# Kernel tuning notes

Hardware: AMD Instinct MI355X
Metric: run time of the kernel (lower is better)

The kernel has to match this reference:

```python
import jax, jax.numpy as jnp
import numpy as np

N_NODES = 50000
N_EDGES = 800000
HIDDEN = 128
HEADS = 8
HEAD_DIM = HIDDEN // HEADS
N_REL = 64
SCALE = np.sqrt(HEAD_DIM).astype(np.float32)


def setup_inputs() -> dict:
    key = jax.random.key(0)
    ks = jax.random.split(key, 12)
    s = 1.0 / np.sqrt(2 * HIDDEN)
    s2 = 1.0 / np.sqrt(HIDDEN)
    return {
        "node_features": jax.random.normal(ks[0], (N_NODES, HIDDEN), jnp.float32),
        "query_embedding": jax.random.normal(ks[1], (1, HIDDEN), jnp.float32),
        "relation_embeddings": jax.random.normal(ks[2], (N_REL, HIDDEN), jnp.float32),
        "Wq": jax.random.uniform(ks[3], (2 * HIDDEN, HIDDEN), jnp.float32, -s, s),
        "bq": jnp.zeros((HIDDEN,), jnp.float32),
        "Wk": jax.random.uniform(ks[4], (2 * HIDDEN, HIDDEN), jnp.float32, -s, s),
        "bk": jnp.zeros((HIDDEN,), jnp.float32),
        "Wv": jax.random.uniform(ks[5], (HIDDEN, HIDDEN), jnp.float32, -s2, s2),
        "bv": jnp.zeros((HIDDEN,), jnp.float32),
        "Wo": jax.random.uniform(ks[6], (HIDDEN, HIDDEN), jnp.float32, -s2, s2),
        "bo": jnp.zeros((HIDDEN,), jnp.float32),
        "edge_index": jax.random.randint(ks[7], (2, N_EDGES), 0, N_NODES, jnp.int64),
        "edge_type": jax.random.randint(ks[8], (N_EDGES,), 0, N_REL, jnp.int64),
    }


def reference(node_features, query_embedding, relation_embeddings,
              Wq, bq, Wk, bk, Wv, bv, Wo, bo, edge_index, edge_type):
    n = node_features.shape[0]
    # expand query to all nodes and concat: [N, 2*hidden]
    q_exp = jnp.broadcast_to(query_embedding, (n, HIDDEN))
    nq = jnp.concatenate([node_features, q_exp], axis=-1)
    q = (nq @ Wq + bq).reshape(n, HEADS, HEAD_DIM)
    k = (nq @ Wk + bk).reshape(n, HEADS, HEAD_DIM)
    v = (node_features @ Wv + bv).reshape(n, HEADS, HEAD_DIM)

    src, dst = edge_index[0], edge_index[1]
    rel_bias = relation_embeddings[edge_type].reshape(-1, HEADS, HEAD_DIM)

    # edge-wise scores [E, heads]
    scores = jnp.sum(q[dst] * (k[src] + rel_bias), axis=-1) / SCALE

    # sparse softmax grouped by dst; torch init of max buffer is 0 -> clamp at 0
    seg_max = jax.ops.segment_max(scores, dst, num_segments=n)
    seg_max = jnp.maximum(seg_max, 0.0)
    exp_s = jnp.exp(scores - seg_max[dst])
    seg_sum = jax.ops.segment_sum(exp_s, dst, num_segments=n)
    attn = exp_s / (seg_sum[dst] + 1e-8)  # [E, heads]

    messages = attn[:, :, None] * v[src]  # [E, heads, head_dim]
    out = jax.ops.segment_sum(messages, dst, num_segments=n)  # [N, heads, head_dim]
    out = out.reshape(n, HIDDEN)
    return out @ Wo + bo
```

## Files before the change

### kernel.cpp

```cpp
#include <hip/hip_runtime.h>
#include <math.h>

#define N_NODES 50000
#define N_EDGES 800000
#define HID 128
#define HEADS 8
#define HDIM 16
#define CNT_BLOCKS 3125
#define QKV_BLOCKS 782

typedef __attribute__((ext_vector_type(8))) short short8;
typedef __attribute__((ext_vector_type(4))) float floatx4;

#if defined(__has_builtin)
#if __has_builtin(__builtin_amdgcn_fdot2_f32_bf16)
#define HAVE_DOT2 1
#endif
#endif
#ifndef HAVE_DOT2
#define HAVE_DOT2 0
#endif

#if HAVE_DOT2
typedef __attribute__((ext_vector_type(2))) __bf16 bf16x2;
__device__ __forceinline__ float dot2acc(unsigned int a, unsigned int b, float c) {
    return __builtin_amdgcn_fdot2_f32_bf16(__builtin_bit_cast(bf16x2, a),
                                           __builtin_bit_cast(bf16x2, b), c, false);
}
#endif

__device__ __forceinline__ float bf_lo(unsigned int d) { return __uint_as_float(d << 16); }
__device__ __forceinline__ float bf_hi(unsigned int d) { return __uint_as_float(d & 0xFFFF0000u); }
__device__ __forceinline__ unsigned short f2bf(float f) {
    unsigned int u = __float_as_uint(f);
    u = (u + 0x7FFFu + ((u >> 16) & 1u)) >> 16;
    return (unsigned short)u;
}
__device__ __forceinline__ unsigned int pack_bf2(float a, float b) {
    return (unsigned int)f2bf(a) | ((unsigned int)f2bf(b) << 16);
}

__global__ __launch_bounds__(256) void prep_count_kernel(
    const float* __restrict__ query, const float* __restrict__ rel,
    const float* __restrict__ Wq, const float* __restrict__ bq,
    const float* __restrict__ Wk, const float* __restrict__ bk,
    const float* __restrict__ Wv, const float* __restrict__ Wo,
    const int* __restrict__ ei,
    unsigned short* __restrict__ Wt, unsigned short* __restrict__ relbf,
    int* __restrict__ counts, int* __restrict__ epos,
    float* __restrict__ bqe, float* __restrict__ bke) {
    int b = blockIdx.x;
    if (b < CNT_BLOCKS) {
        int e = b * 256 + threadIdx.x;
        if (e < N_EDGES) epos[e] = atomicAdd(&counts[ei[N_EDGES + e]], 1);
        return;
    }
    b -= CNT_BLOCKS;
    if (b == 256) {
        int j = threadIdx.x;
        if (j < HID) {
            float aq = bq[j], ak = bk[j];
            for (int i = 0; i < HID; ++i) {
                float qv = query[i];
                aq += qv * Wq[(HID + i) * HID + j];
                ak += qv * Wk[(HID + i) * HID + j];
            }
            bqe[j] = aq;
            bke[j] = ak;
        }
        return;
    }
    int idx = b * 256 + threadIdx.x;
    if (idx < 64 * HID) relbf[idx] = f2bf(rel[idx]);
    int m = idx >> 14;
    int rem = idx & 16383;
    int n = rem >> 7, k = rem & 127;
    const float* W = (m == 0) ? Wq : (m == 1) ? Wk : (m == 2) ? Wv : Wo;
    Wt[idx] = f2bf(W[k * HID + n]);
}

__global__ __launch_bounds__(256) void scan1_kernel(const int* __restrict__ counts,
                                                    int* __restrict__ row_start,
                                                    int* __restrict__ bsums) {
    __shared__ int wsum[4];
    int b = blockIdx.x, tid = threadIdx.x, lane = tid & 63, w = tid >> 6;
    int i0 = b * 1024 + tid * 4;
    int x0 = (i0 + 0 < N_NODES) ? counts[i0 + 0] : 0;
    int x1 = (i0 + 1 < N_NODES) ? counts[i0 + 1] : 0;
    int x2 = (i0 + 2 < N_NODES) ? counts[i0 + 2] : 0;
    int x3 = (i0 + 3 < N_NODES) ? counts[i0 + 3] : 0;
    int t = x0 + x1 + x2 + x3;
    int val = t;
    #pragma unroll
    for (int off = 1; off < 64; off <<= 1) {
        int y = __shfl_up(val, off);
        if (lane >= off) val += y;
    }
    if (lane == 63) wsum[w] = val;
    __syncthreads();
    int wo = 0;
    if (w > 0) wo += wsum[0];
    if (w > 1) wo += wsum[1];
    if (w > 2) wo += wsum[2];
    int excl = wo + val - t;
    if (i0 + 0 < N_NODES) row_start[i0 + 0] = excl;
    if (i0 + 1 < N_NODES) row_start[i0 + 1] = excl + x0;
    if (i0 + 2 < N_NODES) row_start[i0 + 2] = excl + x0 + x1;
    if (i0 + 3 < N_NODES) row_start[i0 + 3] = excl + x0 + x1 + x2;
    if (tid == 255) bsums[b] = wo + val;
}

__global__ __launch_bounds__(256) void scan23_kernel(int* __restrict__ row_start,
                                                     const int* __restrict__ bsums) {
    __shared__ int soff;
    int b = blockIdx.x, tid = threadIdx.x;
    if (tid < 64) {
        int x = (tid < b) ? bsums[tid] : 0;
        #pragma unroll
        for (int off = 32; off > 0; off >>= 1) x += __shfl_down(x, off);
        if (tid == 0) soff = x;
    }
    __syncthreads();
    int off = soff;
    int i0 = b * 1024 + tid * 4;
    if (i0 + 3 < N_NODES) {
        int4* p = (int4*)(row_start + i0);
        int4 v = *p;
        v.x += off; v.y += off; v.z += off; v.w += off;
        *p = v;
    } else {
        for (int j = 0; j < 4; ++j)
            if (i0 + j < N_NODES) row_start[i0 + j] += off;
    }
    if (b == 0 && tid == 0) row_start[N_NODES] = N_EDGES;
}

__global__ __launch_bounds__(256) void qkv_scatter_kernel(
    const float* __restrict__ nf, const unsigned short* __restrict__ Wt,
    const float* __restrict__ bqe, const float* __restrict__ bke, const float* __restrict__ bv,
    const int* __restrict__ ei, const int* __restrict__ et,
    const int* __restrict__ row_start, const int* __restrict__ epos,
    unsigned short* __restrict__ qb16, unsigned short* __restrict__ kv16,
    unsigned int* __restrict__ csr) {
    if (blockIdx.x >= QKV_BLOCKS) {
        int e = (blockIdx.x - QKV_BLOCKS) * 256 + threadIdx.x;
        if (e < N_EDGES) {
            int dst = ei[N_EDGES + e];
            csr[row_start[dst] + epos[e]] = ((unsigned int)et[e] << 18) | (unsigned int)ei[e];
        }
        return;
    }
    int row0 = blockIdx.x * 64;
    int wave = threadIdx.x >> 6;
    int lane = threadIdx.x & 63;
    int col  = lane & 15;
    int quad = lane >> 4;

    short8 afr[4][4];
    #pragma unroll
    for (int t = 0; t < 4; ++t) {
        int arow = row0 + t * 16 + col;
        int asafe = (arow < N_NODES) ? arow : (N_NODES - 1);
        #pragma unroll
        for (int kk = 0; kk < 4; ++kk) {
            const float4* ap = (const float4*)(nf + (size_t)asafe * HID + kk * 32 + quad * 8);
            float4 a0 = ap[0], a1 = ap[1];
            short8 f;
            f[0] = (short)f2bf(a0.x); f[1] = (short)f2bf(a0.y);
            f[2] = (short)f2bf(a0.z); f[3] = (short)f2bf(a0.w);
            f[4] = (short)f2bf(a1.x); f[5] = (short)f2bf(a1.y);
            f[6] = (short)f2bf(a1.z); f[7] = (short)f2bf(a1.w);
            afr[t][kk] = f;
        }
    }

    const float* biases[3] = {bqe, bke, bv};
    #pragma unroll
    for (int m = 0; m < 3; ++m) {
        const unsigned short* W = Wt + (size_t)m * HID * HID;
        #pragma unroll
        for (int nn = 0; nn < 2; ++nn) {
            int n = wave * 2 + nn;
            float b = biases[m][n * 16 + col];
            floatx4 acc[4];
            #pragma unroll
            for (int t = 0; t < 4; ++t) acc[t] = (floatx4){b, b, b, b};
            short8 bfr[4];
            #pragma unroll
            for (int kk = 0; kk < 4; ++kk)
                bfr[kk] = *(const short8*)(W + (size_t)(n * 16 + col) * HID + kk * 32 + quad * 8);
            #pragma unroll
            for (int kk = 0; kk < 4; ++kk)
                #pragma unroll
                for (int t = 0; t < 4; ++t)
                    acc[t] = __builtin_amdgcn_mfma_f32_16x16x32_bf16(afr[t][kk], bfr[kk], acc[t], 0, 0, 0);
            #pragma unroll
            for (int t = 0; t < 4; ++t) {
                #pragma unroll
                for (int i = 0; i < 4; ++i) {
                    int r = row0 + t * 16 + quad * 4 + i;
                    if (r < N_NODES) {
                        int c = n * 16 + col;
                        if (m == 0)      qb16[(size_t)r * HID + c] = f2bf(acc[t][i]);
                        else if (m == 1) kv16[(size_t)r * 256 + c] = f2bf(acc[t][i]);
                        else             kv16[(size_t)r * 256 + 128 + c] = f2bf(acc[t][i]);
                    }
                }
            }
        }
    }
}

__global__ __launch_bounds__(256) void out_mfma_kernel(
    const unsigned short* __restrict__ abuf, const unsigned short* __restrict__ Wot,
    const float* __restrict__ bo, float* __restrict__ out) {
    int row0 = blockIdx.x * 64;
    int wave = threadIdx.x >> 6;
    int lane = threadIdx.x & 63;
    int col  = lane & 15;
    int quad = lane >> 4;

    short8 afr[4][4];
    #pragma unroll
    for (int t = 0; t < 4; ++t) {
        int arow = row0 + t * 16 + col;
        int asafe = (arow < N_NODES) ? arow : (N_NODES - 1);
        #pragma unroll
        for (int kk = 0; kk < 4; ++kk)
            afr[t][kk] = *(const short8*)(abuf + (size_t)asafe * HID + kk * 32 + quad * 8);
    }

    #pragma unroll
    for (int nn = 0; nn < 2; ++nn) {
        int n = wave * 2 + nn;
        float b = bo[n * 16 + col];
        floatx4 acc[4];
        #pragma unroll
        for (int t = 0; t < 4; ++t) acc[t] = (floatx4){b, b, b, b};
        short8 bfr[4];
        #pragma unroll
        for (int kk = 0; kk < 4; ++kk)
            bfr[kk] = *(const short8*)(Wot + (size_t)(n * 16 + col) * HID + kk * 32 + quad * 8);
        #pragma unroll
        for (int kk = 0; kk < 4; ++kk)
            #pragma unroll
            for (int t = 0; t < 4; ++t)
                acc[t] = __builtin_amdgcn_mfma_f32_16x16x32_bf16(afr[t][kk], bfr[kk], acc[t], 0, 0, 0);
        #pragma unroll
        for (int t = 0; t < 4; ++t) {
            #pragma unroll
            for (int i = 0; i < 4; ++i) {
                int r = row0 + t * 16 + quad * 4 + i;
                if (r < N_NODES) out[(size_t)r * HID + n * 16 + col] = acc[t][i];
            }
        }
    }
}

__global__ __launch_bounds__(256) void attn_kernel(
    const unsigned int* __restrict__ qb, const unsigned int* __restrict__ kvu,
    const unsigned int* __restrict__ relu,
    const int* __restrict__ row_start, const unsigned int* __restrict__ csr,
    unsigned int* __restrict__ abuf) {
    __shared__ float lds_acc[2][64][2];
    __shared__ float lds_ssum[2][2][8];
    int slot = threadIdx.x >> 7;
    int wv   = (threadIdx.x >> 6) & 1;
    int node = blockIdx.x * 2 + slot;
    int lane = threadIdx.x & 63;
    int h = lane & 7;
    int hd = lane >> 3;
    int rs = row_start[node];
    int deg = row_start[node + 1] - rs;

    const uint4* qp = (const uint4*)(qb + (unsigned)node * 64 + h * 8);
    uint4 qa = qp[0], qc = qp[1];
#if !HAVE_DOT2
    float qf0 = bf_lo(qa.x), qf1 = bf_hi(qa.x), qf2 = bf_lo(qa.y), qf3 = bf_hi(qa.y);
    float qf4 = bf_lo(qa.z), qf5 = bf_hi(qa.z), qf6 = bf_lo(qa.w), qf7 = bf_hi(qa.w);
    float qf8 = bf_lo(qc.x), qf9 = bf_hi(qc.x), qf10 = bf_lo(qc.y), qf11 = bf_hi(qc.y);
    float qf12 = bf_lo(qc.z), qf13 = bf_hi(qc.z), qf14 = bf_lo(qc.w), qf15 = bf_hi(qc.w);
#endif

    int myel0 = wv * 8 + (lane >> 3);
    float ssum = 0.0f, accx = 0.0f, accy = 0.0f;
    for (int base = 0; base < deg; base += 16) {
        int el = base + myel0;
        unsigned int pw = 0u;
        if (el < deg) {
            unsigned int pk = csr[rs + el];
            unsigned int src = pk & 0x3FFFF;
            unsigned int etv = pk >> 18;
            const uint4* kp = (const uint4*)(kvu + (src << 7) + h * 8);
            uint4 ka = kp[0], kb = kp[1];
            const uint4* rp = (const uint4*)(relu + (etv << 6) + h * 8);
            uint4 ra = rp[0], rb = rp[1];
            float s;
#if HAVE_DOT2
            float s0 = dot2acc(qa.x, ka.x, 0.0f);
            float s1 = dot2acc(qa.y, ka.y, 0.0f);
            float s2 = dot2acc(qa.z, ka.z, 0.0f);
            float s3 = dot2acc(qa.w, ka.w, 0.0f);
            s0 = dot2acc(qc.x, kb.x, s0);
            s1 = dot2acc(qc.y, kb.y, s1);
            s2 = dot2acc(qc.z, kb.z, s2);
            s3 = dot2acc(qc.w, kb.w, s3);
            s0 = dot2acc(qa.x, ra.x, s0);
            s1 = dot2acc(qa.y, ra.y, s1);
            s2 = dot2acc(qa.z, ra.z, s2);
            s3 = dot2acc(qa.w, ra.w, s3);
            s0 = dot2acc(qc.x, rb.x, s0);
            s1 = dot2acc(qc.y, rb.y, s1);
            s2 = dot2acc(qc.z, rb.z, s2);
            s3 = dot2acc(qc.w, rb.w, s3);
            s = (s0 + s1) + (s2 + s3);
#else
            float s0 = qf0 * (bf_lo(ka.x) + bf_lo(ra.x)) + qf4 * (bf_lo(ka.z) + bf_lo(ra.z))
                     + qf8 * (bf_lo(kb.x) + bf_lo(rb.x)) + qf12 * (bf_lo(kb.z) + bf_lo(rb.z));
            float s1 = qf1 * (bf_hi(ka.x) + bf_hi(ra.x)) + qf5 * (bf_hi(ka.z) + bf_hi(ra.z))
                     + qf9 * (bf_hi(kb.x) + bf_hi(rb.x)) + qf13 * (bf_hi(kb.z) + bf_hi(rb.z));
            float s2 = qf2 * (bf_lo(ka.y) + bf_lo(ra.y)) + qf6 * (bf_lo(ka.w) + bf_lo(ra.w))
                     + qf10 * (bf_lo(kb.y) + bf_lo(rb.y)) + qf14 * (bf_lo(kb.w) + bf_lo(rb.w));
            float s3 = qf3 * (bf_hi(ka.y) + bf_hi(ra.y)) + qf7 * (bf_hi(ka.w) + bf_hi(ra.w))
                     + qf11 * (bf_hi(kb.y) + bf_hi(rb.y)) + qf15 * (bf_hi(kb.w) + bf_hi(rb.w));
            s = (s0 + s1) + (s2 + s3);
#endif
            float w = __expf(s * 0.25f);
            unsigned int wb = (unsigned int)f2bf(w);
            w = __uint_as_float(wb << 16);
            ssum += w;
            pw = (wb << 16) | src;
        }
        #pragma unroll
        for (int j = 0; j < 8; ++j) {
            unsigned int pj = __shfl(pw, j * 8 + hd);
            float wj = bf_hi(pj);
            unsigned int sj = pj & 0xFFFFu;
            unsigned int vp = kvu[(sj << 7) + 64 + lane];
            accx += wj * bf_lo(vp);
            accy += wj * bf_hi(vp);
        }
    }
    #pragma unroll
    for (int off = 8; off < 64; off <<= 1) ssum += __shfl_xor(ssum, off);

    if (lane < 8) lds_ssum[slot][wv][lane] = ssum;
    if (wv == 1) { lds_acc[slot][lane][0] = accx; lds_acc[slot][lane][1] = accy; }
    __syncthreads();
    if (wv == 0) {
        accx += lds_acc[slot][lane][0];
        accy += lds_acc[slot][lane][1];
        float stot = lds_ssum[slot][0][hd] + lds_ssum[slot][1][hd];
        float inv = 1.0f / (stot + 1e-8f);
        abuf[(unsigned)node * 64 + lane] = pack_bf2(accx * inv, accy * inv);
    }
}

extern "C" void kernel_launch(void* const* d_in, const int* in_sizes, int n_in,
                              void* d_out, int out_size, void* d_ws, size_t ws_size,
                              hipStream_t stream) {
    const float* nf    = (const float*)d_in[0];
    const float* query = (const float*)d_in[1];
    const float* rel   = (const float*)d_in[2];
    const float* Wq    = (const float*)d_in[3];
    const float* bq    = (const float*)d_in[4];
    const float* Wk    = (const float*)d_in[5];
    const float* bk    = (const float*)d_in[6];
    const float* Wv    = (const float*)d_in[7];
    const float* bv    = (const float*)d_in[8];
    const float* Wo    = (const float*)d_in[9];
    const float* bo    = (const float*)d_in[10];
    const int*   ei    = (const int*)d_in[11];
    const int*   et    = (const int*)d_in[12];
    float* out = (float*)d_out;

    char* ws = (char*)d_ws;
    unsigned short* qb16 = (unsigned short*)ws; ws += (size_t)N_NODES * HID * 2;
    unsigned short* kv16 = (unsigned short*)ws; ws += (size_t)N_NODES * 256 * 2;
    unsigned int* abuf   = (unsigned int*)ws;   ws += (size_t)N_NODES * 64 * 4;
    float* bqe           = (float*)ws;          ws += 128 * 4;
    float* bke           = (float*)ws;          ws += 128 * 4;
    int* row_start       = (int*)ws;            ws += (size_t)(N_NODES + 4) * 4;
    int* counts          = (int*)ws;            ws += (size_t)N_NODES * 4;
    int* epos            = (int*)ws;            ws += (size_t)N_EDGES * 4;
    int* bsums           = (int*)ws;            ws += 64 * 4;
    unsigned int* csr    = (unsigned int*)ws;   ws += (size_t)N_EDGES * 4;
    unsigned short* Wt   = (unsigned short*)ws; ws += (size_t)4 * HID * HID * 2;
    unsigned short* relbf = (unsigned short*)ws; ws += (size_t)64 * HID * 2;

    const int SCAN_BLOCKS = (N_NODES + 1023) / 1024;

    hipMemsetAsync(counts, 0, (size_t)N_NODES * 4, stream);
    prep_count_kernel<<<CNT_BLOCKS + 257, 256, 0, stream>>>(
        query, rel, Wq, bq, Wk, bk, Wv, Wo, ei, Wt, relbf, counts, epos, bqe, bke);
    scan1_kernel<<<SCAN_BLOCKS, 256, 0, stream>>>(counts, row_start, bsums);
    scan23_kernel<<<SCAN_BLOCKS, 256, 0, stream>>>(row_start, bsums);
    qkv_scatter_kernel<<<QKV_BLOCKS + CNT_BLOCKS, 256, 0, stream>>>(
        nf, Wt, bqe, bke, bv, ei, et, row_start, epos, qb16, kv16, csr);
    attn_kernel<<<N_NODES / 2, 256, 0, stream>>>(
        (const unsigned int*)qb16, (const unsigned int*)kv16,
        (const unsigned int*)relbf, row_start, csr, abuf);
    out_mfma_kernel<<<QKV_BLOCKS, 256, 0, stream>>>(
        (const unsigned short*)abuf, Wt + (size_t)3 * HID * HID, bo, out);
}
```

Baseline: 246.0 us.

## Fuse preprocessing, counting, scan and CSR scatter into one cooperative kernel

Replaces the memset, prep/count, two scan kernels and the qkv/scatter kernel with a single cooperative persistent kernel that uses grid-wide syncs between phases. The scan now has each block sum all earlier counts itself instead of running a second pass. The attention kernel gives each wave its own node instead of splitting one node across two waves, and prefetches the next CSR entry, which drops the LDS reduction and __syncthreads. This cuts launch overheads and intermediate kernel boundaries, at the cost of grid syncs, occupancy limits from the launch bound, and a redundant prefix sum in each scan block.

```diff
diff --git a/kernel.cpp b/kernel.cpp
--- a/kernel.cpp
+++ b/kernel.cpp
@@ -1,5 +1,8 @@
 #include <hip/hip_runtime.h>
+#include <hip/hip_cooperative_groups.h>
 #include <math.h>
+
+namespace cg = cooperative_groups;
 
 #define N_NODES 50000
 #define N_EDGES 800000
@@ -8,6 +11,7 @@
 #define HDIM 16
 #define CNT_BLOCKS 3125
 #define QKV_BLOCKS 782
+#define SCAN_BLOCKS 49
 
 typedef __attribute__((ext_vector_type(8))) short short8;
 typedef __attribute__((ext_vector_type(4))) float floatx4;
@@ -40,219 +44,167 @@
     return (unsigned int)f2bf(a) | ((unsigned int)f2bf(b) << 16);
 }
 
-__global__ __launch_bounds__(256) void prep_count_kernel(
+__global__ __launch_bounds__(256, 4) void mega_kernel(
     const float* __restrict__ query, const float* __restrict__ rel,
     const float* __restrict__ Wq, const float* __restrict__ bq,
     const float* __restrict__ Wk, const float* __restrict__ bk,
     const float* __restrict__ Wv, const float* __restrict__ Wo,
-    const int* __restrict__ ei,
+    const float* __restrict__ bv,
+    const float* __restrict__ nf, const int* __restrict__ ei, const int* __restrict__ et,
     unsigned short* __restrict__ Wt, unsigned short* __restrict__ relbf,
-    int* __restrict__ counts, int* __restrict__ epos,
-    float* __restrict__ bqe, float* __restrict__ bke) {
-    int b = blockIdx.x;
-    if (b < CNT_BLOCKS) {
-        int e = b * 256 + threadIdx.x;
-        if (e < N_EDGES) epos[e] = atomicAdd(&counts[ei[N_EDGES + e]], 1);
-        return;
-    }
-    b -= CNT_BLOCKS;
-    if (b == 256) {
-        int j = threadIdx.x;
-        if (j < HID) {
-            float aq = bq[j], ak = bk[j];
-            for (int i = 0; i < HID; ++i) {
-                float qv = query[i];
-                aq += qv * Wq[(HID + i) * HID + j];
-                ak += qv * Wk[(HID + i) * HID + j];
+    float* __restrict__ bqe, float* __restrict__ bke,
+    int* __restrict__ counts, int* __restrict__ epos, int* __restrict__ row_start,
+    unsigned int* __restrict__ csr, unsigned short* __restrict__ qb16,
+    unsigned short* __restrict__ kv16) {
+    cg::grid_group gridg = cg::this_grid();
+    __shared__ int smem[264];
+    int nb = gridDim.x;
+    int b0 = blockIdx.x;
+    int tid = threadIdx.x;
+
+    for (int v = b0; v < 258; v += nb) {
+        if (v < 256) {
+            int idx = v * 256 + tid;
+            if (idx < N_NODES) counts[idx] = 0;
+            if (idx < 64 * HID) relbf[idx] = f2bf(rel[idx]);
+            int m = idx >> 14;
+            int rem = idx & 16383;
+            int n = rem >> 7, k = rem & 127;
+            const float* W = (m == 0) ? Wq : (m == 1) ? Wk : (m == 2) ? Wv : Wo;
+            Wt[idx] = f2bf(W[k * HID + n]);
+        } else {
+            const float* W  = (v == 256) ? Wq : Wk;
+            const float* bb = (v == 256) ? bq : bk;
+            float* dst      = (v == 256) ? bqe : bke;
+            int j = tid & 127;
+            int half = tid >> 7;
+            float a = 0.0f;
+            int i0 = half * 64;
+            for (int i = 0; i < 64; ++i) a += query[i0 + i] * W[(HID + i0 + i) * HID + j];
+            float* fred = (float*)smem;
+            fred[tid] = a;
+            __syncthreads();
+            if (half == 0) dst[j] = fred[j] + fred[128 + j] + bb[j];
+            __syncthreads();
+        }
+    }
+    gridg.sync();
+
+    for (int v = b0; v < QKV_BLOCKS + CNT_BLOCKS; v += nb) {
+        if (v >= QKV_BLOCKS) {
+            int e = (v - QKV_BLOCKS) * 256 + tid;
+            if (e < N_EDGES) epos[e] = atomicAdd(&counts[ei[N_EDGES + e]], 1);
+            continue;
+        }
+        int row0 = v * 64;
+        int wave = tid >> 6;
+        int lane = tid & 63;
+        int col  = lane & 15;
+        int quad = lane >> 4;
+
+        short8 afr[4][4];
+        #pragma unroll
+        for (int t = 0; t < 4; ++t) {
+            int arow = row0 + t * 16 + col;
+            int asafe = (arow < N_NODES) ? arow : (N_NODES - 1);
+            #pragma unroll
+            for (int kk = 0; kk < 4; ++kk) {
+                const float4* ap = (const float4*)(nf + (size_t)asafe * HID + kk * 32 + quad * 8);
+                float4 a0 = ap[0], a1 = ap[1];
+                short8 f;
+                f[0] = (short)f2bf(a0.x); f[1] = (short)f2bf(a0.y);
+                f[2] = (short)f2bf(a0.z); f[3] = (short)f2bf(a0.w);
+                f[4] = (short)f2bf(a1.x); f[5] = (short)f2bf(a1.y);
+                f[6] = (short)f2bf(a1.z); f[7] = (short)f2bf(a1.w);
+                afr[t][kk] = f;
             }
-            bqe[j] = aq;
-            bke[j] = ak;
-        }
-        return;
-    }
-    int idx = b * 256 + threadIdx.x;
-    if (idx < 64 * HID) relbf[idx] = f2bf(rel[idx]);
-    int m = idx >> 14;
-    int rem = idx & 16383;
-    int n = rem >> 7, k = rem & 127;
-    const float* W = (m == 0) ? Wq : (m == 1) ? Wk : (m == 2) ? Wv : Wo;
-    Wt[idx] = f2bf(W[k * HID + n]);
-}
-
-__global__ __launch_bounds__(256) void scan1_kernel(const int* __restrict__ counts,
-                                                    int* __restrict__ row_start,
-                                                    int* __restrict__ bsums) {
-    __shared__ int wsum[4];
-    int b = blockIdx.x, tid = threadIdx.x, lane = tid & 63, w = tid >> 6;
-    int i0 = b * 1024 + tid * 4;
-    int x0 = (i0 + 0 < N_NODES) ? counts[i0 + 0] : 0;
-    int x1 = (i0 + 1 < N_NODES) ? counts[i0 + 1] : 0;
-    int x2 = (i0 + 2 < N_NODES) ? counts[i0 + 2] : 0;
-    int x3 = (i0 + 3 < N_NODES) ? counts[i0 + 3] : 0;
-    int t = x0 + x1 + x2 + x3;
-    int val = t;
-    #pragma unroll
-    for (int off = 1; off < 64; off <<= 1) {
-        int y = __shfl_up(val, off);
-        if (lane >= off) val += y;
-    }
-    if (lane == 63) wsum[w] = val;
-    __syncthreads();
-    int wo = 0;
-    if (w > 0) wo += wsum[0];
-    if (w > 1) wo += wsum[1];
-    if (w > 2) wo += wsum[2];
-    int excl = wo + val - t;
-    if (i0 + 0 < N_NODES) row_start[i0 + 0] = excl;
-    if (i0 + 1 < N_NODES) row_start[i0 + 1] = excl + x0;
-    if (i0 + 2 < N_NODES) row_start[i0 + 2] = excl + x0 + x1;
-    if (i0 + 3 < N_NODES) row_start[i0 + 3] = excl + x0 + x1 + x2;
-    if (tid == 255) bsums[b] = wo + val;
-}
-
-__global__ __launch_bounds__(256) void scan23_kernel(int* __restrict__ row_start,
-                                                     const int* __restrict__ bsums) {
-    __shared__ int soff;
-    int b = blockIdx.x, tid = threadIdx.x;
-    if (tid < 64) {
-        int x = (tid < b) ? bsums[tid] : 0;
-        #pragma unroll
-        for (int off = 32; off > 0; off >>= 1) x += __shfl_down(x, off);
-        if (tid == 0) soff = x;
-    }
-    __syncthreads();
-    int off = soff;
-    int i0 = b * 1024 + tid * 4;
-    if (i0 + 3 < N_NODES) {
-        int4* p = (int4*)(row_start + i0);
-        int4 v = *p;
-        v.x += off; v.y += off; v.z += off; v.w += off;
-        *p = v;
-    } else {
-        for (int j = 0; j < 4; ++j)
-            if (i0 + j < N_NODES) row_start[i0 + j] += off;
-    }
-    if (b == 0 && tid == 0) row_start[N_NODES] = N_EDGES;
-}
-
-__global__ __launch_bounds__(256) void qkv_scatter_kernel(
-    const float* __restrict__ nf, const unsigned short* __restrict__ Wt,
-    const float* __restrict__ bqe, const float* __restrict__ bke, const float* __restrict__ bv,
-    const int* __restrict__ ei, const int* __restrict__ et,
-    const int* __restrict__ row_start, const int* __restrict__ epos,
-    unsigned short* __restrict__ qb16, unsigned short* __restrict__ kv16,
-    unsigned int* __restrict__ csr) {
-    if (blockIdx.x >= QKV_BLOCKS) {
-        int e = (blockIdx.x - QKV_BLOCKS) * 256 + threadIdx.x;
+        }
+        const float* biases[3] = {bqe, bke, bv};
+        #pragma unroll
+        for (int m = 0; m < 3; ++m) {
+            const unsigned short* W = Wt + (size_t)m * HID * HID;
+            #pragma unroll
+            for (int nn = 0; nn < 2; ++nn) {
+                int n = wave * 2 + nn;
+                float b = biases[m][n * 16 + col];
+                floatx4 acc[4];
+                #pragma unroll
+                for (int t = 0; t < 4; ++t) acc[t] = (floatx4){b, b, b, b};
+                short8 bfr[4];
+                #pragma unroll
+                for (int kk = 0; kk < 4; ++kk)
+                    bfr[kk] = *(const short8*)(W + (size_t)(n * 16 + col) * HID + kk * 32 + quad * 8);
+                #pragma unroll
+                for (int kk = 0; kk < 4; ++kk)
+                    #pragma unroll
+                    for (int t = 0; t < 4; ++t)
+                        acc[t] = __builtin_amdgcn_mfma_f32_16x16x32_bf16(afr[t][kk], bfr[kk], acc[t], 0, 0, 0);
+                #pragma unroll
+                for (int t = 0; t < 4; ++t) {
+                    #pragma unroll
+                    for (int i = 0; i < 4; ++i) {
+                        int r = row0 + t * 16 + quad * 4 + i;
+                        if (r < N_NODES) {
+                            int c = n * 16 + col;
+                            if (m == 0)      qb16[(size_t)r * HID + c] = f2bf(acc[t][i]);
+                            else if (m == 1) kv16[(size_t)r * 256 + c] = f2bf(acc[t][i]);
+                            else             kv16[(size_t)r * 256 + 128 + c] = f2bf(acc[t][i]);
+                        }
+                    }
+                }
+            }
+        }
+    }
+    gridg.sync();
+
+    for (int v = b0; v < SCAN_BLOCKS; v += nb) {
+        int limit = v << 10;
+        int part = 0;
+        for (int i = tid; i < limit; i += 256) part += counts[i];
+        smem[tid] = part;
+        __syncthreads();
+        #pragma unroll
+        for (int s2 = 128; s2 > 0; s2 >>= 1) {
+            if (tid < s2) smem[tid] += smem[tid + s2];
+            __syncthreads();
+        }
+        int offset = smem[0];
+        __syncthreads();
+
+        int lane = tid & 63, w = tid >> 6;
+        int i0 = (v << 10) + tid * 4;
+        int x0 = (i0 + 0 < N_NODES) ? counts[i0 + 0] : 0;
+        int x1 = (i0 + 1 < N_NODES) ? counts[i0 + 1] : 0;
+        int x2 = (i0 + 2 < N_NODES) ? counts[i0 + 2] : 0;
+        int x3 = (i0 + 3 < N_NODES) ? counts[i0 + 3] : 0;
+        int t = x0 + x1 + x2 + x3;
+        int val = t;
+        #pragma unroll
+        for (int off = 1; off < 64; off <<= 1) {
+            int y = __shfl_up(val, off);
+            if (lane >= off) val += y;
+        }
+        if (lane == 63) smem[256 + w] = val;
+        __syncthreads();
+        int wo = 0;
+        if (w > 0) wo += smem[256 + 0];
+        if (w > 1) wo += smem[256 + 1];
+        if (w > 2) wo += smem[256 + 2];
+        int excl = offset + wo + val - t;
+        if (i0 + 0 < N_NODES) row_start[i0 + 0] = excl;
+        if (i0 + 1 < N_NODES) row_start[i0 + 1] = excl + x0;
+        if (i0 + 2 < N_NODES) row_start[i0 + 2] = excl + x0 + x1;
+        if (i0 + 3 < N_NODES) row_start[i0 + 3] = excl + x0 + x1 + x2;
+        if (v == 0 && tid == 0) row_start[N_NODES] = N_EDGES;
+        __syncthreads();
+    }
+    gridg.sync();
+
+    for (int v = b0; v < CNT_BLOCKS; v += nb) {
+        int e = v * 256 + tid;
         if (e < N_EDGES) {
             int dst = ei[N_EDGES + e];
             csr[row_start[dst] + epos[e]] = ((unsigned int)et[e] << 18) | (unsigned int)ei[e];
-        }
-        return;
-    }
-    int row0 = blockIdx.x * 64;
-    int wave = threadIdx.x >> 6;
-    int lane = threadIdx.x & 63;
-    int col  = lane & 15;
-    int quad = lane >> 4;
-
-    short8 afr[4][4];
-    #pragma unroll
-    for (int t = 0; t < 4; ++t) {
-        int arow = row0 + t * 16 + col;
-        int asafe = (arow < N_NODES) ? arow : (N_NODES - 1);
-        #pragma unroll
-        for (int kk = 0; kk < 4; ++kk) {
-            const float4* ap = (const float4*)(nf + (size_t)asafe * HID + kk * 32 + quad * 8);
-            float4 a0 = ap[0], a1 = ap[1];
-            short8 f;
-            f[0] = (short)f2bf(a0.x); f[1] = (short)f2bf(a0.y);
-            f[2] = (short)f2bf(a0.z); f[3] = (short)f2bf(a0.w);
-            f[4] = (short)f2bf(a1.x); f[5] = (short)f2bf(a1.y);
-            f[6] = (short)f2bf(a1.z); f[7] = (short)f2bf(a1.w);
-            afr[t][kk] = f;
-        }
-    }
-
-    const float* biases[3] = {bqe, bke, bv};
-    #pragma unroll
-    for (int m = 0; m < 3; ++m) {
-        const unsigned short* W = Wt + (size_t)m * HID * HID;
-        #pragma unroll
-        for (int nn = 0; nn < 2; ++nn) {
-            int n = wave * 2 + nn;
-            float b = biases[m][n * 16 + col];
-            floatx4 acc[4];
-            #pragma unroll
-            for (int t = 0; t < 4; ++t) acc[t] = (floatx4){b, b, b, b};
-            short8 bfr[4];
-            #pragma unroll
-            for (int kk = 0; kk < 4; ++kk)
-                bfr[kk] = *(const short8*)(W + (size_t)(n * 16 + col) * HID + kk * 32 + quad * 8);
-            #pragma unroll
-            for (int kk = 0; kk < 4; ++kk)
-                #pragma unroll
-                for (int t = 0; t < 4; ++t)
-                    acc[t] = __builtin_amdgcn_mfma_f32_16x16x32_bf16(afr[t][kk], bfr[kk], acc[t], 0, 0, 0);
-            #pragma unroll
-            for (int t = 0; t < 4; ++t) {
-                #pragma unroll
-                for (int i = 0; i < 4; ++i) {
-                    int r = row0 + t * 16 + quad * 4 + i;
-                    if (r < N_NODES) {
-                        int c = n * 16 + col;
-                        if (m == 0)      qb16[(size_t)r * HID + c] = f2bf(acc[t][i]);
-                        else if (m == 1) kv16[(size_t)r * 256 + c] = f2bf(acc[t][i]);
-                        else             kv16[(size_t)r * 256 + 128 + c] = f2bf(acc[t][i]);
-                    }
-                }
-            }
-        }
-    }
-}
-
-__global__ __launch_bounds__(256) void out_mfma_kernel(
-    const unsigned short* __restrict__ abuf, const unsigned short* __restrict__ Wot,
-    const float* __restrict__ bo, float* __restrict__ out) {
-    int row0 = blockIdx.x * 64;
-    int wave = threadIdx.x >> 6;
-    int lane = threadIdx.x & 63;
-    int col  = lane & 15;
-    int quad = lane >> 4;
-
-    short8 afr[4][4];
-    #pragma unroll
-    for (int t = 0; t < 4; ++t) {
-        int arow = row0 + t * 16 + col;
-        int asafe = (arow < N_NODES) ? arow : (N_NODES - 1);
-        #pragma unroll
-        for (int kk = 0; kk < 4; ++kk)
-            afr[t][kk] = *(const short8*)(abuf + (size_t)asafe * HID + kk * 32 + quad * 8);
-    }
-
-    #pragma unroll
-    for (int nn = 0; nn < 2; ++nn) {
-        int n = wave * 2 + nn;
-        float b = bo[n * 16 + col];
-        floatx4 acc[4];
-        #pragma unroll
-        for (int t = 0; t < 4; ++t) acc[t] = (floatx4){b, b, b, b};
-        short8 bfr[4];
-        #pragma unroll
-        for (int kk = 0; kk < 4; ++kk)
-            bfr[kk] = *(const short8*)(Wot + (size_t)(n * 16 + col) * HID + kk * 32 + quad * 8);
-        #pragma unroll
-        for (int kk = 0; kk < 4; ++kk)
-            #pragma unroll
-            for (int t = 0; t < 4; ++t)
-                acc[t] = __builtin_amdgcn_mfma_f32_16x16x32_bf16(afr[t][kk], bfr[kk], acc[t], 0, 0, 0);
-        #pragma unroll
-        for (int t = 0; t < 4; ++t) {
-            #pragma unroll
-            for (int i = 0; i < 4; ++i) {
-                int r = row0 + t * 16 + quad * 4 + i;
-                if (r < N_NODES) out[(size_t)r * HID + n * 16 + col] = acc[t][i];
-            }
         }
     }
 }
@@ -262,11 +214,7 @@
     const unsigned int* __restrict__ relu,
     const int* __restrict__ row_start, const unsigned int* __restrict__ csr,
     unsigned int* __restrict__ abuf) {
-    __shared__ float lds_acc[2][64][2];
-    __shared__ float lds_ssum[2][2][8];
-    int slot = threadIdx.x >> 7;
-    int wv   = (threadIdx.x >> 6) & 1;
-    int node = blockIdx.x * 2 + slot;
+    int node = blockIdx.x * 4 + (threadIdx.x >> 6);
     int lane = threadIdx.x & 63;
     int h = lane & 7;
     int hd = lane >> 3;
@@ -282,13 +230,15 @@
     float qf12 = bf_lo(qc.z), qf13 = bf_hi(qc.z), qf14 = bf_lo(qc.w), qf15 = bf_hi(qc.w);
 #endif
 
-    int myel0 = wv * 8 + (lane >> 3);
+    int myel = hd;
+    unsigned int pk = (myel < deg) ? csr[rs + myel] : 0u;
     float ssum = 0.0f, accx = 0.0f, accy = 0.0f;
-    for (int base = 0; base < deg; base += 16) {
-        int el = base + myel0;
+    for (int base = 0; base < deg; base += 8) {
+        int el = base + myel;
+        int eln = el + 8;
+        unsigned int pk_next = (eln < deg) ? csr[rs + eln] : 0u;
         unsigned int pw = 0u;
         if (el < deg) {
-            unsigned int pk = csr[rs + el];
             unsigned int src = pk & 0x3FFFF;
             unsigned int etv = pk >> 18;
             const uint4* kp = (const uint4*)(kvu + (src << 7) + h * 8);
@@ -327,8 +277,7 @@
 #endif
             float w = __expf(s * 0.25f);
             unsigned int wb = (unsigned int)f2bf(w);
-            w = __uint_as_float(wb << 16);
-            ssum += w;
+            ssum += __uint_as_float(wb << 16);
             pw = (wb << 16) | src;
         }
         #pragma unroll
@@ -340,19 +289,57 @@
             accx += wj * bf_lo(vp);
             accy += wj * bf_hi(vp);
         }
+        pk = pk_next;
     }
     #pragma unroll
     for (int off = 8; off < 64; off <<= 1) ssum += __shfl_xor(ssum, off);
-
-    if (lane < 8) lds_ssum[slot][wv][lane] = ssum;
-    if (wv == 1) { lds_acc[slot][lane][0] = accx; lds_acc[slot][lane][1] = accy; }
-    __syncthreads();
-    if (wv == 0) {
-        accx += lds_acc[slot][lane][0];
-        accy += lds_acc[slot][lane][1];
-        float stot = lds_ssum[slot][0][hd] + lds_ssum[slot][1][hd];
-        float inv = 1.0f / (stot + 1e-8f);
-        abuf[(unsigned)node * 64 + lane] = pack_bf2(accx * inv, accy * inv);
+    float inv = 1.0f / (__shfl(ssum, hd) + 1e-8f);
+    abuf[(unsigned)node * 64 + lane] = pack_bf2(accx * inv, accy * inv);
+}
+
+__global__ __launch_bounds__(256) void out_mfma_kernel(
+    const unsigned short* __restrict__ abuf, const unsigned short* __restrict__ Wot,
+    const float* __restrict__ bo, float* __restrict__ out) {
+    int row0 = blockIdx.x * 64;
+    int wave = threadIdx.x >> 6;
+    int lane = threadIdx.x & 63;
+    int col  = lane & 15;
+    int quad = lane >> 4;
+
+    short8 afr[4][4];
+    #pragma unroll
+    for (int t = 0; t < 4; ++t) {
+        int arow = row0 + t * 16 + col;
+        int asafe = (arow < N_NODES) ? arow : (N_NODES - 1);
+        #pragma unroll
+        for (int kk = 0; kk < 4; ++kk)
+            afr[t][kk] = *(const short8*)(abuf + (size_t)asafe * HID + kk * 32 + quad * 8);
+    }
+
+    #pragma unroll
+    for (int nn = 0; nn < 2; ++nn) {
+        int n = wave * 2 + nn;
+        float b = bo[n * 16 + col];
+        floatx4 acc[4];
+        #pragma unroll
+        for (int t = 0; t < 4; ++t) acc[t] = (floatx4){b, b, b, b};
+        short8 bfr[4];
+        #pragma unroll
+        for (int kk = 0; kk < 4; ++kk)
+            bfr[kk] = *(const short8*)(Wot + (size_t)(n * 16 + col) * HID + kk * 32 + quad * 8);
+        #pragma unroll
+        for (int kk = 0; kk < 4; ++kk)
+            #pragma unroll
+            for (int t = 0; t < 4; ++t)
+                acc[t] = __builtin_amdgcn_mfma_f32_16x16x32_bf16(afr[t][kk], bfr[kk], acc[t], 0, 0, 0);
+        #pragma unroll
+        for (int t = 0; t < 4; ++t) {
+            #pragma unroll
+            for (int i = 0; i < 4; ++i) {
+                int r = row0 + t * 16 + quad * 4 + i;
+                if (r < N_NODES) out[(size_t)r * HID + n * 16 + col] = acc[t][i];
+            }
+        }
     }
 }
 
@@ -383,21 +370,29 @@
     int* row_start       = (int*)ws;            ws += (size_t)(N_NODES + 4) * 4;
     int* counts          = (int*)ws;            ws += (size_t)N_NODES * 4;
     int* epos            = (int*)ws;            ws += (size_t)N_EDGES * 4;
-    int* bsums           = (int*)ws;            ws += 64 * 4;
     unsigned int* csr    = (unsigned int*)ws;   ws += (size_t)N_EDGES * 4;
     unsigned short* Wt   = (unsigned short*)ws; ws += (size_t)4 * HID * HID * 2;
     unsigned short* relbf = (unsigned short*)ws; ws += (size_t)64 * HID * 2;
 
-    const int SCAN_BLOCKS = (N_NODES + 1023) / 1024;
-
-    hipMemsetAsync(counts, 0, (size_t)N_NODES * 4, stream);
-    prep_count_kernel<<<CNT_BLOCKS + 257, 256, 0, stream>>>(
-        query, rel, Wq, bq, Wk, bk, Wv, Wo, ei, Wt, relbf, counts, epos, bqe, bke);
-    scan1_kernel<<<SCAN_BLOCKS, 256, 0, stream>>>(counts, row_start, bsums);
-    scan23_kernel<<<SCAN_BLOCKS, 256, 0, stream>>>(row_start, bsums);
-    qkv_scatter_kernel<<<QKV_BLOCKS + CNT_BLOCKS, 256, 0, stream>>>(
-        nf, Wt, bqe, bke, bv, ei, et, row_start, epos, qb16, kv16, csr);
-    attn_kernel<<<N_NODES / 2, 256, 0, stream>>>(
+    int bpc = 0;
+    if (hipOccupancyMaxActiveBlocksPerMultiprocessor(&bpc, mega_kernel, 256, 0) != hipSuccess || bpc <= 0)
+        bpc = 1;
+    if (bpc > 4) bpc = 4;
+    int mgrid = 256 * bpc;
+
+    void* margs[] = {
+        (void*)&query, (void*)&rel,
+        (void*)&Wq, (void*)&bq, (void*)&Wk, (void*)&bk,
+        (void*)&Wv, (void*)&Wo, (void*)&bv,
+        (void*)&nf, (void*)&ei, (void*)&et,
+        (void*)&Wt, (void*)&relbf,
+        (void*)&bqe, (void*)&bke,
+        (void*)&counts, (void*)&epos, (void*)&row_start,
+        (void*)&csr, (void*)&qb16, (void*)&kv16,
+    };
+    hipLaunchCooperativeKernel((void*)mega_kernel, dim3(mgrid), dim3(256), margs, 0, stream);
+
+    attn_kernel<<<N_NODES / 4, 256, 0, stream>>>(
         (const unsigned int*)qb16, (const unsigned int*)kv16,
         (const unsigned int*)relbf, row_start, csr, abuf);
     out_mfma_kernel<<<QKV_BLOCKS, 256, 0, stream>>>(
```

Result: slower. 490.2 us (+99.2%).
